# Kernel optimization log

Measured on AMD Instinct MI355X. Metric: run time of the kernel, lower is better.

The kernel has to match this reference:

```python
import jax, jax.numpy as jnp
import numpy as np
import math

B, S, DIM = 2, 2048, 2048
H, KV = 32, 8
HD = DIM // H          # 64
REP = H // KV          # 4
NEG = -1e9


def setup_inputs() -> dict:
    key = jax.random.key(0)
    ks = jax.random.split(key, 8)
    x = jax.random.normal(ks[0], (B, S, DIM), dtype=jnp.float32)
    # RoPE frequencies: theta = 10000^{-2i/d}, angles = pos * theta
    inv_freq = 1.0 / (10000.0 ** (jnp.arange(0, HD, 2, dtype=jnp.float32) / HD))  # [HD/2]
    angles = jnp.arange(S, dtype=jnp.float32)[:, None] * inv_freq[None, :]        # [S, HD/2]
    freqs_cos = jnp.cos(angles)
    freqs_sin = jnp.sin(angles)
    # additive causal mask [1,1,S,S]
    causal = jnp.tril(jnp.ones((S, S), dtype=bool))
    mask = jnp.where(causal, 0.0, NEG).astype(jnp.float32)[None, None]
    sc = 1.0 / math.sqrt(DIM)
    wq = jax.random.normal(ks[1], (DIM, H * HD), dtype=jnp.float32) * sc
    wk = jax.random.normal(ks[2], (DIM, KV * HD), dtype=jnp.float32) * sc
    wv = jax.random.normal(ks[3], (DIM, KV * HD), dtype=jnp.float32) * sc
    wo = jax.random.normal(ks[4], (H * HD, DIM), dtype=jnp.float32) * sc
    return {"x": x, "freqs_cos": freqs_cos, "freqs_sin": freqs_sin,
            "mask": mask, "wq": wq, "wk": wk, "wv": wv, "wo": wo}


def _rope(t, cos, sin):
    # t: [B,S,nh,HD]; interleaved (even, odd) pairs == view_as_complex layout
    te, to = t[..., 0::2], t[..., 1::2]
    c = cos[None, :, None, :]  # [1,S,1,HD/2]
    s = sin[None, :, None, :]
    oe = te * c - to * s
    oo = te * s + to * c
    return jnp.stack([oe, oo], axis=-1).reshape(t.shape)


def reference(x, freqs_cos, freqs_sin, mask, wq, wk, wv, wo):
    b, s, _ = x.shape
    q = (x @ wq).reshape(b, s, H, HD)
    k = (x @ wk).reshape(b, s, KV, HD)
    v = (x @ wv).reshape(b, s, KV, HD)
    q = _rope(q, freqs_cos, freqs_sin)
    k = _rope(k, freqs_cos, freqs_sin)
    # GQA without materializing repeat_interleave: group q heads by kv head
    # repeat_interleave maps query head h -> kv head h // REP
    qg = q.transpose(0, 2, 1, 3).reshape(b, KV, REP, s, HD)  # [B,KV,REP,S,HD]
    kg = k.transpose(0, 2, 1, 3)                              # [B,KV,S,HD]
    vg = v.transpose(0, 2, 1, 3)
    scores = jnp.einsum('bgrqd,bgkd->bgrqk', qg, kg) / math.sqrt(HD)
    scores = scores + mask[:, :, None]                        # [1,1,1,S,S] broadcast
    attn = jax.nn.softmax(scores, axis=-1)
    out = jnp.einsum('bgrqk,bgkd->bgrqd', attn, vg)           # [B,KV,REP,S,HD]
    out = out.reshape(b, H, s, HD).transpose(0, 2, 1, 3).reshape(b, s, H * HD)
    return out @ wo
```

## Files before the change

### kernel.cpp

```cpp
#include <hip/hip_runtime.h>
#include <hip/hip_bf16.h>

#define B_ 2
#define S_ 2048
#define DIM_ 2048
#define H_ 32
#define KV_ 8
#define HD_ 64

typedef __bf16 bf16x8 __attribute__((ext_vector_type(8)));
typedef __bf16 bf16x4 __attribute__((ext_vector_type(4)));
typedef float f32x4 __attribute__((ext_vector_type(4)));
typedef float f32x16 __attribute__((ext_vector_type(16)));
typedef unsigned u32x2 __attribute__((ext_vector_type(2)));

#define GLOAD16(gp, lp) __builtin_amdgcn_global_load_lds( \
    (const __attribute__((address_space(1))) void*)(gp),  \
    (__attribute__((address_space(3))) void*)(lp), 16, 0, 0)

__global__ __launch_bounds__(256) void cast_f32_bf16_v4(const float* __restrict__ in,
                                                        __bf16* __restrict__ out, int n4) {
    int i = blockIdx.x * 256 + threadIdx.x;
    if (i >= n4) return;
    float4 v = ((const float4*)in)[i];
    bf16x4 o;
    o[0] = (__bf16)v.x; o[1] = (__bf16)v.y; o[2] = (__bf16)v.z; o[3] = (__bf16)v.w;
    ((bf16x4*)out)[i] = o;
}

__global__ __launch_bounds__(256) void transpose_all_t(const float* __restrict__ wq,
                                                       const float* __restrict__ wk,
                                                       const float* __restrict__ wv,
                                                       const float* __restrict__ wo,
                                                       __bf16* __restrict__ wqkv_t,
                                                       __bf16* __restrict__ wo_t) {
    __shared__ float t[32][33];
    const int bk = blockIdx.x * 32, bn = blockIdx.y * 32;
    const int tx = threadIdx.x & 31, ty = threadIdx.x >> 5;
    const float* W; __bf16* Wt; int N, src;
    if (blockIdx.z == 0) {
        Wt = wqkv_t;
        if (bn < 2048)      { W = wq; N = 2048; src = bn; }
        else if (bn < 2560) { W = wk; N = 512;  src = bn - 2048; }
        else                { W = wv; N = 512;  src = bn - 2560; }
    } else {
        if (bn >= 2048) return;
        Wt = wo_t; W = wo; N = 2048; src = bn;
    }
#pragma unroll
    for (int i = 0; i < 4; i++)
        t[ty * 4 + i][tx] = W[(size_t)(bk + ty * 4 + i) * N + src + tx];
    __syncthreads();
#pragma unroll
    for (int i = 0; i < 4; i++)
        Wt[(size_t)(bn + ty * 4 + i) * 2048 + bk + tx] = (__bf16)t[tx][ty * 4 + i];
}

__global__ __launch_bounds__(512, 2)
void gemm256_qkv(const __bf16* __restrict__ A, const __bf16* __restrict__ Bt,
                 __bf16* __restrict__ q_bf, __bf16* __restrict__ k_bf,
                 __bf16* __restrict__ vt_bf,
                 const float* __restrict__ fc, const float* __restrict__ fs) {
    __shared__ __align__(16) char smem[131072];
    char* lA = smem;
    char* lB = smem + 65536;
    const int K = DIM_;
    const int tid = threadIdx.x, lane = tid & 63, wid = tid >> 6;
    const int wr2 = wid >> 2, wc2 = wid & 3;
    const int fr = lane & 15, fg = lane >> 4;
    const long i0 = (long)blockIdx.x * 256;
    const long j0 = (long)blockIdx.y * 256;

    const int r0 = tid >> 3;
    const int cc = ((tid & 7) ^ (r0 & 7)) * 8;
    const __bf16* pA = A + (i0 + r0) * (long)K + cc;
    const __bf16* pB = Bt + (j0 + r0) * (long)K + cc;
    const int NT = K >> 6;

    f32x4 acc[8][4] = {};

#define STGA(h, kt, buf) do { \
    GLOAD16(pA + (long)((h) * 128) * K + (kt) * 64,      lA + (buf) * 32768 + (h) * 16384 + tid * 16); \
    GLOAD16(pA + (long)((h) * 128 + 64) * K + (kt) * 64, lA + (buf) * 32768 + (h) * 16384 + 8192 + tid * 16); } while (0)
#define STGB(h, kt, buf) do { \
    GLOAD16(pB + (long)((h) * 128) * K + (kt) * 64,      lB + (buf) * 32768 + (h) * 16384 + tid * 16); \
    GLOAD16(pB + (long)((h) * 128 + 64) * K + (kt) * 64, lB + (buf) * 32768 + (h) * 16384 + 8192 + tid * 16); } while (0)

    STGA(0, 0, 0); STGB(0, 0, 0); STGB(1, 0, 0); STGA(1, 0, 0);

    for (int kt = 0; kt < NT; ++kt) {
        const int cur = kt & 1, nxt = cur ^ 1;
        const bool nl = (kt + 1 < NT);
        const char* cA = lA + cur * 32768;
        const char* cB = lB + cur * 32768;
        bf16x8 af[4], bfv[4];

        auto rdA = [&](int mf, int ks) -> bf16x8 {
            int row = wr2 * 128 + mf * 16 + fr;
            return *(const bf16x8*)(cA + row * 128 + (((ks << 2) | fg) ^ (row & 7)) * 16);
        };
        auto rdB = [&](int nf, int ks) -> bf16x8 {
            int row = wc2 * 64 + nf * 16 + fr;
            return *(const bf16x8*)(cB + row * 128 + (((ks << 2) | fg) ^ (row & 7)) * 16);
        };

        if (nl) { STGA(0, kt + 1, nxt); STGB(0, kt + 1, nxt); }
        if (nl) asm volatile("s_waitcnt vmcnt(4)" ::: "memory");
        else    asm volatile("s_waitcnt vmcnt(0)" ::: "memory");
        __builtin_amdgcn_s_barrier();
        asm volatile("" ::: "memory");
#pragma unroll
        for (int nf = 0; nf < 4; nf++) bfv[nf] = rdB(nf, 0);
#pragma unroll
        for (int mf = 0; mf < 4; mf++) af[mf] = rdA(mf, 0);
        __builtin_amdgcn_s_setprio(1);
#pragma unroll
        for (int mf = 0; mf < 4; mf++)
#pragma unroll
            for (int nf = 0; nf < 4; nf++)
                acc[mf][nf] = __builtin_amdgcn_mfma_f32_16x16x32_bf16(af[mf], bfv[nf], acc[mf][nf], 0, 0, 0);
        __builtin_amdgcn_s_setprio(0);
        __builtin_amdgcn_s_barrier();

#pragma unroll
        for (int mf = 0; mf < 4; mf++) af[mf] = rdA(4 + mf, 0);
        if (nl) { STGB(1, kt + 1, nxt); STGA(1, kt + 1, nxt); }
        __builtin_amdgcn_s_barrier();
        __builtin_amdgcn_s_setprio(1);
#pragma unroll
        for (int mf = 0; mf < 4; mf++)
#pragma unroll
            for (int nf = 0; nf < 4; nf++)
                acc[4 + mf][nf] = __builtin_amdgcn_mfma_f32_16x16x32_bf16(af[mf], bfv[nf], acc[4 + mf][nf], 0, 0, 0);
        __builtin_amdgcn_s_setprio(0);
        __builtin_amdgcn_s_barrier();

#pragma unroll
        for (int nf = 0; nf < 4; nf++) bfv[nf] = rdB(nf, 1);
#pragma unroll
        for (int mf = 0; mf < 4; mf++) af[mf] = rdA(mf, 1);
        __builtin_amdgcn_s_barrier();
        __builtin_amdgcn_s_setprio(1);
#pragma unroll
        for (int mf = 0; mf < 4; mf++)
#pragma unroll
            for (int nf = 0; nf < 4; nf++)
                acc[mf][nf] = __builtin_amdgcn_mfma_f32_16x16x32_bf16(af[mf], bfv[nf], acc[mf][nf], 0, 0, 0);
        __builtin_amdgcn_s_setprio(0);
        __builtin_amdgcn_s_barrier();

#pragma unroll
        for (int mf = 0; mf < 4; mf++) af[mf] = rdA(4 + mf, 1);
        __builtin_amdgcn_s_barrier();
        __builtin_amdgcn_s_setprio(1);
#pragma unroll
        for (int mf = 0; mf < 4; mf++)
#pragma unroll
            for (int nf = 0; nf < 4; nf++)
                acc[4 + mf][nf] = __builtin_amdgcn_mfma_f32_16x16x32_bf16(af[mf], bfv[nf], acc[4 + mf][nf], 0, 0, 0);
        __builtin_amdgcn_s_setprio(0);
        __builtin_amdgcn_s_barrier();
    }
#undef STGA
#undef STGB

    const long col0 = j0 + wc2 * 64;
    if (j0 < 2048) {
#pragma unroll
        for (int mf = 0; mf < 8; mf++)
#pragma unroll
            for (int nf = 0; nf < 4; nf++)
#pragma unroll
                for (int j = 0; j < 4; j++) {
                    long row = i0 + wr2 * 128 + mf * 16 + fg * 4 + j;
                    q_bf[row * 2048 + col0 + nf * 16 + fr] = (__bf16)acc[mf][nf][j];
                }
    } else if (j0 < 2560) {
#pragma unroll
        for (int mf = 0; mf < 8; mf++)
#pragma unroll
            for (int nf = 0; nf < 4; nf++) {
                const int kd = (int)(col0 + nf * 16 + fr - 2048);
                const int i_ = (kd & 63) >> 1;
                const float sgn = (fr & 1) ? 1.0f : -1.0f;
#pragma unroll
                for (int j = 0; j < 4; j++) {
                    long row = i0 + wr2 * 128 + mf * 16 + fg * 4 + j;
                    int s = (int)(row & (S_ - 1));
                    float cv = fc[s * 32 + i_], sv = fs[s * 32 + i_];
                    float v = acc[mf][nf][j];
                    float p = __shfl_xor(v, 1, 64);
                    k_bf[row * 512 + kd] = (__bf16)(v * cv + sgn * sv * p);
                }
            }
    } else {
#pragma unroll
        for (int mf = 0; mf < 8; mf++)
#pragma unroll
            for (int nf = 0; nf < 4; nf++) {
                const int vd = (int)(col0 + nf * 16 + fr - 2560);
                long row0 = i0 + wr2 * 128 + mf * 16 + fg * 4;
                int b = (int)(row0 >> 11);
                int s = (int)(row0 & (S_ - 1));
                bf16x4 pk;
#pragma unroll
                for (int j = 0; j < 4; j++) pk[j] = (__bf16)acc[mf][nf][j];
                *(bf16x4*)(vt_bf + ((size_t)(b * KV_ + (vd >> 6)) * HD_ + (vd & 63)) * S_ + s) = pk;
            }
    }
}

__global__ __launch_bounds__(512, 2)
void gemm256_o(const __bf16* __restrict__ A, const __bf16* __restrict__ Bt,
               float* __restrict__ C) {
    __shared__ __align__(16) char smem[98304];
    char* lA = smem;
    char* lB = smem + 32768;
    const int K = DIM_;
    const int tid = threadIdx.x, lane = tid & 63, wid = tid >> 6;
    const int wr2 = wid >> 2, wc2 = wid & 3;
    const int fr = lane & 15, fg = lane >> 4;
    const int id = blockIdx.x;
    const long i0 = (long)(id >> 3) * 128;
    const long j0 = (long)(id & 7) * 256;

    const int r0 = tid >> 3;
    const int cc = ((tid & 7) ^ (r0 & 7)) * 8;
    const __bf16* pA = A + (i0 + r0) * (long)K + cc;
    const __bf16* pB = Bt + (j0 + r0) * (long)K + cc;
    const int NT = K >> 6;

    f32x4 acc[4][4] = {};

#define STG(kt, buf) do { \
    GLOAD16(pA + (long)(kt) * 64,                  lA + (buf) * 16384 + tid * 16); \
    GLOAD16(pA + (long)64 * K + (long)(kt) * 64,   lA + (buf) * 16384 + 8192 + tid * 16); \
    GLOAD16(pB + (long)(kt) * 64,                  lB + (buf) * 32768 + tid * 16); \
    GLOAD16(pB + (long)64 * K + (long)(kt) * 64,   lB + (buf) * 32768 + 8192 + tid * 16); \
    GLOAD16(pB + (long)128 * K + (long)(kt) * 64,  lB + (buf) * 32768 + 16384 + tid * 16); \
    GLOAD16(pB + (long)192 * K + (long)(kt) * 64,  lB + (buf) * 32768 + 24576 + tid * 16); } while (0)

    STG(0, 0);

    for (int kt = 0; kt < NT; ++kt) {
        const int cur = kt & 1, nxt = cur ^ 1;
        const bool nl = (kt + 1 < NT);
        const char* cA = lA + cur * 16384;
        const char* cB = lB + cur * 32768;

        if (nl) STG(kt + 1, nxt);
        if (nl) asm volatile("s_waitcnt vmcnt(6)" ::: "memory");
        else    asm volatile("s_waitcnt vmcnt(0)" ::: "memory");
        __builtin_amdgcn_s_barrier();
        asm volatile("" ::: "memory");

        bf16x8 af[4], bfv[4];
#pragma unroll
        for (int ks = 0; ks < 2; ks++) {
#pragma unroll
            for (int nf = 0; nf < 4; nf++) {
                int row = wc2 * 64 + nf * 16 + fr;
                bfv[nf] = *(const bf16x8*)(cB + row * 128 + (((ks << 2) | fg) ^ (row & 7)) * 16);
            }
#pragma unroll
            for (int mf = 0; mf < 4; mf++) {
                int row = wr2 * 64 + mf * 16 + fr;
                af[mf] = *(const bf16x8*)(cA + row * 128 + (((ks << 2) | fg) ^ (row & 7)) * 16);
            }
            __builtin_amdgcn_s_setprio(1);
#pragma unroll
            for (int mf = 0; mf < 4; mf++)
#pragma unroll
                for (int nf = 0; nf < 4; nf++)
                    acc[mf][nf] = __builtin_amdgcn_mfma_f32_16x16x32_bf16(af[mf], bfv[nf], acc[mf][nf], 0, 0, 0);
            __builtin_amdgcn_s_setprio(0);
        }
        __builtin_amdgcn_s_barrier();
    }
#undef STG

#pragma unroll
    for (int mf = 0; mf < 4; mf++)
#pragma unroll
        for (int nf = 0; nf < 4; nf++)
#pragma unroll
            for (int j = 0; j < 4; j++) {
                long row = i0 + wr2 * 64 + mf * 16 + fg * 4 + j;
                long col = j0 + wc2 * 64 + nf * 16 + fr;
                C[row * 2048 + col] = acc[mf][nf][j];
            }
}

__global__ __launch_bounds__(256, 4)
void attn_fwd(const __bf16* __restrict__ Q, const __bf16* __restrict__ Kb,
              const __bf16* __restrict__ Vt, __bf16* __restrict__ O,
              const float* __restrict__ fc, const float* __restrict__ fs) {
    extern __shared__ __align__(16) char smem[];
    __bf16* lK  = (__bf16*)smem;
    __bf16* lVt = (__bf16*)(smem + 16384);

    const int tid = threadIdx.x;
    const int lane = tid & 63;
    const int wid = tid >> 6;
    const int ln = lane & 31;
    const int hi = lane >> 5;

    const int id = blockIdx.x;
    const int g = id & 7;
    const int r = id >> 3;
    const int chunk = 15 - (r >> 3);
    const int hb = r & 7;
    const int b = hb & 1;
    const int h = g * 4 + (hb >> 1);
    const int QS = H_ * HD_, KS = KV_ * HD_;
    const float K2 = 0.18033688011112042f;
    const float mK = 8.0f * K2;

    const __bf16* Kbse = Kb + (size_t)(b * S_) * KS + g * HD_;
    const __bf16* Vbse = Vt + (size_t)((b * KV_ + g) * HD_) * S_;

    bf16x8 onesf;
#pragma unroll
    for (int j = 0; j < 8; j++) onesf[j] = (__bf16)1.0f;

    const int c0 = tid, c1 = tid + 256;
    const int kr0 = c0 & 63, kd0 = c0 >> 6;
    const int kr1 = c1 & 63, kd1 = c1 >> 6;
    const __bf16* Ksrc0 = Kbse + (size_t)kr0 * KS + kd0 * 8;
    const __bf16* Ksrc1 = Kbse + (size_t)kr1 * KS + kd1 * 8;
    const __bf16* Vsrc0 = Vbse + (size_t)kr0 * S_ + kd0 * 8;
    const __bf16* Vsrc1 = Vbse + (size_t)kr1 * S_ + kd1 * 8;

    auto stage = [&](int t, int buf) {
        GLOAD16(Ksrc0 + (size_t)t * 64 * KS, lK + buf * 4096 + c0 * 8);
        GLOAD16(Ksrc1 + (size_t)t * 64 * KS, lK + buf * 4096 + c1 * 8);
        GLOAD16(Vsrc0 + t * 64,              lVt + buf * 4096 + c0 * 8);
        GLOAD16(Vsrc1 + t * 64,              lVt + buf * 4096 + c1 * 8);
    };

    const int q0w = chunk * 128 + wid * 32;
    const int qrow = q0w + ln;
    const int nt = 2 * chunk + 2;
    const int nkv_w = (q0w >> 6) + 1;

    const __bf16* Qb = Q + (size_t)(b * S_ + qrow) * QS + h * HD_;
    const float* cz = fc + (size_t)qrow * 32;
    const float* sz = fs + (size_t)qrow * 32;
    bf16x8 qf[4];
#pragma unroll
    for (int kk = 0; kk < 4; kk++) {
        bf16x8 raw = *(const bf16x8*)(Qb + kk * 16 + hi * 8);
#pragma unroll
        for (int p = 0; p < 4; p++) {
            const int i = kk * 8 + hi * 4 + p;
            float cv = cz[i], sv = sz[i];
            float e = (float)raw[2 * p], o = (float)raw[2 * p + 1];
            qf[kk][2 * p]     = (__bf16)(e * cv - o * sv);
            qf[kk][2 * p + 1] = (__bf16)(e * sv + o * cv);
        }
    }

    f32x16 o0 = {}, o1 = {}, o2 = {};

    stage(0, 0);
    __syncthreads();

    for (int t = 0; t < nt; t++) {
        if (t + 1 < nt) stage(t + 1, (t + 1) & 1);
        if (t < nkv_w) {
            const char* lKc = (const char*)(lK + (t & 1) * 4096);
            const char* lVc = (const char*)(lVt + (t & 1) * 4096);
            const int p0 = t * 64;

            f32x16 s0 = {}, s1 = {};
            __builtin_amdgcn_s_setprio(1);
#pragma unroll
            for (int kk = 0; kk < 4; kk++) {
                bf16x8 ka = *(const bf16x8*)(lKc + (kk * 2 + hi) * 1024 + ln * 16);
                s0 = __builtin_amdgcn_mfma_f32_32x32x16_bf16(ka, qf[kk], s0, 0, 0, 0);
            }
#pragma unroll
            for (int kk = 0; kk < 4; kk++) {
                bf16x8 ka = *(const bf16x8*)(lKc + (kk * 2 + hi) * 1024 + (32 + ln) * 16);
                s1 = __builtin_amdgcn_mfma_f32_32x32x16_bf16(ka, qf[kk], s1, 0, 0, 0);
            }
            __builtin_amdgcn_s_setprio(0);

            if (t == nkv_w - 1) {
#pragma unroll
                for (int rr = 0; rr < 16; rr++) {
                    int crow = (rr & 3) + 8 * (rr >> 2) + 4 * hi;
                    if (p0 + crow > qrow)      s0[rr] = -1e30f;
                    if (p0 + 32 + crow > qrow) s1[rr] = -1e30f;
                }
            }

#pragma unroll
            for (int rr = 0; rr < 16; rr++) {
                s0[rr] = exp2f(s0[rr] * K2 - mK);
                s1[rr] = exp2f(s1[rr] * K2 - mK);
            }

            __builtin_amdgcn_s_setprio(1);
#pragma unroll
            for (int c = 0; c < 2; c++) {
                const f32x16& pe = c ? s1 : s0;
                unsigned w[4][2];
#pragma unroll
                for (int gi = 0; gi < 4; gi++)
#pragma unroll
                    for (int p = 0; p < 2; p++) {
                        unsigned short lo = __builtin_bit_cast(unsigned short, (__bf16)pe[4 * gi + 2 * p]);
                        unsigned short hp = __builtin_bit_cast(unsigned short, (__bf16)pe[4 * gi + 2 * p + 1]);
                        w[gi][p] = (unsigned)lo | ((unsigned)hp << 16);
                    }
                unsigned pw0[4], pw1[4];
#pragma unroll
                for (int p = 0; p < 2; p++) {
                    u32x2 ra = __builtin_amdgcn_permlane32_swap(w[0][p], w[1][p], false, false);
                    pw0[p] = ra[0]; pw0[2 + p] = ra[1];
                    u32x2 rb = __builtin_amdgcn_permlane32_swap(w[2][p], w[3][p], false, false);
                    pw1[p] = rb[0]; pw1[2 + p] = rb[1];
                }
                bf16x8 pa0 = __builtin_bit_cast(bf16x8, *(uint4*)pw0);
                bf16x8 pa1 = __builtin_bit_cast(bf16x8, *(uint4*)pw1);
#pragma unroll
                for (int half = 0; half < 2; half++) {
                    const int ks = 2 * c + half;
                    bf16x8 pa = half ? pa1 : pa0;
                    bf16x8 va0 = *(const bf16x8*)(lVc + (ks * 2 + hi) * 1024 + ln * 16);
                    bf16x8 va1 = *(const bf16x8*)(lVc + (ks * 2 + hi) * 1024 + (32 + ln) * 16);
                    o0 = __builtin_amdgcn_mfma_f32_32x32x16_bf16(va0, pa, o0, 0, 0, 0);
                    o1 = __builtin_amdgcn_mfma_f32_32x32x16_bf16(va1, pa, o1, 0, 0, 0);
                    o2 = __builtin_amdgcn_mfma_f32_32x32x16_bf16(onesf, pa, o2, 0, 0, 0);
                }
            }
            __builtin_amdgcn_s_setprio(0);
        }
        __syncthreads();
    }

    const float inv = 1.0f / o2[0];
    __bf16* Oq = O + (size_t)(b * S_ + qrow) * QS + h * HD_;
#pragma unroll
    for (int db = 0; db < 2; db++) {
        const f32x16& oo = db ? o1 : o0;
#pragma unroll
        for (int gi = 0; gi < 4; gi++) {
            bf16x4 pk;
#pragma unroll
            for (int j = 0; j < 4; j++) pk[j] = (__bf16)(oo[4 * gi + j] * inv);
            *(bf16x4*)(Oq + db * 32 + 8 * gi + 4 * hi) = pk;
        }
    }
}

extern "C" void kernel_launch(void* const* d_in, const int* in_sizes, int n_in,
                              void* d_out, int out_size, void* d_ws, size_t ws_size,
                              hipStream_t stream) {
    const float* x  = (const float*)d_in[0];
    const float* fc = (const float*)d_in[1];
    const float* fs = (const float*)d_in[2];
    const float* wq = (const float*)d_in[4];
    const float* wk = (const float*)d_in[5];
    const float* wv = (const float*)d_in[6];
    const float* wo = (const float*)d_in[7];
    float* out = (float*)d_out;

    const size_t N0 = (size_t)B_ * S_ * DIM_;
    const size_t N1 = (size_t)B_ * S_ * H_ * HD_;
    const size_t N2 = (size_t)B_ * S_ * KV_ * HD_;
    const size_t N3 = (size_t)DIM_ * H_ * HD_;
    const size_t N4 = (size_t)DIM_ * KV_ * HD_;

    __bf16* x_bf = (__bf16*)d_ws;
    __bf16* q_bf = x_bf + N0;
    __bf16* k_bf = q_bf + N1;
    __bf16* vt_bf = k_bf + N2;
    __bf16* wqkv_t = vt_bf + N2;
    __bf16* wo_t = wqkv_t + N3 + 2 * N4;
    __bf16* ao_bf = x_bf;

    cast_f32_bf16_v4<<<dim3(N0 / 4 / 256), 256, 0, stream>>>(x, x_bf, (int)(N0 / 4));
    transpose_all_t<<<dim3(64, 96, 2), 256, 0, stream>>>(wq, wk, wv, wo, wqkv_t, wo_t);

    gemm256_qkv<<<dim3(16, 12), 512, 0, stream>>>(x_bf, wqkv_t, q_bf, k_bf, vt_bf, fc, fs);

    attn_fwd<<<dim3(1024), 256, 32768, stream>>>(q_bf, k_bf, vt_bf, ao_bf, fc, fs);

    gemm256_o<<<dim3(256), 512, 0, stream>>>(ao_bf, wo_t, out);
}
```

Measured before the change: 197.2 us.

## Load K/V tiles directly from global memory into registers in attention

Removes the LDS double-buffered staging of K and V tiles in the attention kernel. Each wave now loads its K and V MFMA operands straight from global memory into registers, so there are no block-wide barriers and each wave only loops over its own causal range. The four waves in a block share a KV head and read the same K/V rows, so this duplicates global and L2 traffic and exposes load latency without an explicit prefetch pipeline. In exchange it drops the shared-memory allocation, which may raise occupancy.

```diff
diff --git a/kernel.cpp b/kernel.cpp
--- a/kernel.cpp
+++ b/kernel.cpp
@@ -295,10 +295,6 @@
 void attn_fwd(const __bf16* __restrict__ Q, const __bf16* __restrict__ Kb,
               const __bf16* __restrict__ Vt, __bf16* __restrict__ O,
               const float* __restrict__ fc, const float* __restrict__ fs) {
-    extern __shared__ __align__(16) char smem[];
-    __bf16* lK  = (__bf16*)smem;
-    __bf16* lVt = (__bf16*)(smem + 16384);
-
     const int tid = threadIdx.x;
     const int lane = tid & 63;
     const int wid = tid >> 6;
@@ -316,31 +312,13 @@
     const float K2 = 0.18033688011112042f;
     const float mK = 8.0f * K2;
 
-    const __bf16* Kbse = Kb + (size_t)(b * S_) * KS + g * HD_;
-    const __bf16* Vbse = Vt + (size_t)((b * KV_ + g) * HD_) * S_;
-
-    bf16x8 onesf;
-#pragma unroll
-    for (int j = 0; j < 8; j++) onesf[j] = (__bf16)1.0f;
-
-    const int c0 = tid, c1 = tid + 256;
-    const int kr0 = c0 & 63, kd0 = c0 >> 6;
-    const int kr1 = c1 & 63, kd1 = c1 >> 6;
-    const __bf16* Ksrc0 = Kbse + (size_t)kr0 * KS + kd0 * 8;
-    const __bf16* Ksrc1 = Kbse + (size_t)kr1 * KS + kd1 * 8;
-    const __bf16* Vsrc0 = Vbse + (size_t)kr0 * S_ + kd0 * 8;
-    const __bf16* Vsrc1 = Vbse + (size_t)kr1 * S_ + kd1 * 8;
-
-    auto stage = [&](int t, int buf) {
-        GLOAD16(Ksrc0 + (size_t)t * 64 * KS, lK + buf * 4096 + c0 * 8);
-        GLOAD16(Ksrc1 + (size_t)t * 64 * KS, lK + buf * 4096 + c1 * 8);
-        GLOAD16(Vsrc0 + t * 64,              lVt + buf * 4096 + c0 * 8);
-        GLOAD16(Vsrc1 + t * 64,              lVt + buf * 4096 + c1 * 8);
-    };
+    const __bf16* Kl0 = Kb + (size_t)(b * S_ + ln) * KS + g * HD_ + hi * 8;
+    const __bf16* Kl1 = Kl0 + (size_t)32 * KS;
+    const __bf16* Vl0 = Vt + ((size_t)(b * KV_ + g) * HD_ + ln) * S_ + hi * 8;
+    const __bf16* Vl1 = Vl0 + (size_t)32 * S_;
 
     const int q0w = chunk * 128 + wid * 32;
     const int qrow = q0w + ln;
-    const int nt = 2 * chunk + 2;
     const int nkv_w = (q0w >> 6) + 1;
 
     const __bf16* Qb = Q + (size_t)(b * S_ + qrow) * QS + h * HD_;
@@ -360,84 +338,87 @@
         }
     }
 
+    bf16x8 onesf;
+#pragma unroll
+    for (int j = 0; j < 8; j++) onesf[j] = (__bf16)1.0f;
+
     f32x16 o0 = {}, o1 = {}, o2 = {};
 
-    stage(0, 0);
-    __syncthreads();
-
-    for (int t = 0; t < nt; t++) {
-        if (t + 1 < nt) stage(t + 1, (t + 1) & 1);
-        if (t < nkv_w) {
-            const char* lKc = (const char*)(lK + (t & 1) * 4096);
-            const char* lVc = (const char*)(lVt + (t & 1) * 4096);
-            const int p0 = t * 64;
-
-            f32x16 s0 = {}, s1 = {};
-            __builtin_amdgcn_s_setprio(1);
-#pragma unroll
-            for (int kk = 0; kk < 4; kk++) {
-                bf16x8 ka = *(const bf16x8*)(lKc + (kk * 2 + hi) * 1024 + ln * 16);
-                s0 = __builtin_amdgcn_mfma_f32_32x32x16_bf16(ka, qf[kk], s0, 0, 0, 0);
-            }
-#pragma unroll
-            for (int kk = 0; kk < 4; kk++) {
-                bf16x8 ka = *(const bf16x8*)(lKc + (kk * 2 + hi) * 1024 + (32 + ln) * 16);
-                s1 = __builtin_amdgcn_mfma_f32_32x32x16_bf16(ka, qf[kk], s1, 0, 0, 0);
-            }
-            __builtin_amdgcn_s_setprio(0);
-
-            if (t == nkv_w - 1) {
-#pragma unroll
-                for (int rr = 0; rr < 16; rr++) {
-                    int crow = (rr & 3) + 8 * (rr >> 2) + 4 * hi;
-                    if (p0 + crow > qrow)      s0[rr] = -1e30f;
-                    if (p0 + 32 + crow > qrow) s1[rr] = -1e30f;
+    for (int t = 0; t < nkv_w; t++) {
+        const int p0 = t * 64;
+
+        bf16x8 ka0[4], ka1[4];
+#pragma unroll
+        for (int kk = 0; kk < 4; kk++) {
+            ka0[kk] = *(const bf16x8*)(Kl0 + (size_t)p0 * KS + kk * 16);
+            ka1[kk] = *(const bf16x8*)(Kl1 + (size_t)p0 * KS + kk * 16);
+        }
+
+        f32x16 s0 = {}, s1 = {};
+        __builtin_amdgcn_s_setprio(1);
+#pragma unroll
+        for (int kk = 0; kk < 4; kk++)
+            s0 = __builtin_amdgcn_mfma_f32_32x32x16_bf16(ka0[kk], qf[kk], s0, 0, 0, 0);
+#pragma unroll
+        for (int kk = 0; kk < 4; kk++)
+            s1 = __builtin_amdgcn_mfma_f32_32x32x16_bf16(ka1[kk], qf[kk], s1, 0, 0, 0);
+        __builtin_amdgcn_s_setprio(0);
+
+        bf16x8 va[4][2];
+#pragma unroll
+        for (int ks = 0; ks < 4; ks++) {
+            va[ks][0] = *(const bf16x8*)(Vl0 + p0 + ks * 16);
+            va[ks][1] = *(const bf16x8*)(Vl1 + p0 + ks * 16);
+        }
+
+        if (t == nkv_w - 1) {
+#pragma unroll
+            for (int rr = 0; rr < 16; rr++) {
+                int crow = (rr & 3) + 8 * (rr >> 2) + 4 * hi;
+                if (p0 + crow > qrow)      s0[rr] = -1e30f;
+                if (p0 + 32 + crow > qrow) s1[rr] = -1e30f;
+            }
+        }
+
+#pragma unroll
+        for (int rr = 0; rr < 16; rr++) {
+            s0[rr] = exp2f(s0[rr] * K2 - mK);
+            s1[rr] = exp2f(s1[rr] * K2 - mK);
+        }
+
+        __builtin_amdgcn_s_setprio(1);
+#pragma unroll
+        for (int c = 0; c < 2; c++) {
+            const f32x16& pe = c ? s1 : s0;
+            unsigned w[4][2];
+#pragma unroll
+            for (int gi = 0; gi < 4; gi++)
+#pragma unroll
+                for (int p = 0; p < 2; p++) {
+                    unsigned short lo = __builtin_bit_cast(unsigned short, (__bf16)pe[4 * gi + 2 * p]);
+                    unsigned short hp = __builtin_bit_cast(unsigned short, (__bf16)pe[4 * gi + 2 * p + 1]);
+                    w[gi][p] = (unsigned)lo | ((unsigned)hp << 16);
                 }
-            }
-
-#pragma unroll
-            for (int rr = 0; rr < 16; rr++) {
-                s0[rr] = exp2f(s0[rr] * K2 - mK);
-                s1[rr] = exp2f(s1[rr] * K2 - mK);
-            }
-
-            __builtin_amdgcn_s_setprio(1);
-#pragma unroll
-            for (int c = 0; c < 2; c++) {
-                const f32x16& pe = c ? s1 : s0;
-                unsigned w[4][2];
-#pragma unroll
-                for (int gi = 0; gi < 4; gi++)
-#pragma unroll
-                    for (int p = 0; p < 2; p++) {
-                        unsigned short lo = __builtin_bit_cast(unsigned short, (__bf16)pe[4 * gi + 2 * p]);
-                        unsigned short hp = __builtin_bit_cast(unsigned short, (__bf16)pe[4 * gi + 2 * p + 1]);
-                        w[gi][p] = (unsigned)lo | ((unsigned)hp << 16);
-                    }
-                unsigned pw0[4], pw1[4];
-#pragma unroll
-                for (int p = 0; p < 2; p++) {
-                    u32x2 ra = __builtin_amdgcn_permlane32_swap(w[0][p], w[1][p], false, false);
-                    pw0[p] = ra[0]; pw0[2 + p] = ra[1];
-                    u32x2 rb = __builtin_amdgcn_permlane32_swap(w[2][p], w[3][p], false, false);
-                    pw1[p] = rb[0]; pw1[2 + p] = rb[1];
-                }
-                bf16x8 pa0 = __builtin_bit_cast(bf16x8, *(uint4*)pw0);
-                bf16x8 pa1 = __builtin_bit_cast(bf16x8, *(uint4*)pw1);
-#pragma unroll
-                for (int half = 0; half < 2; half++) {
-                    const int ks = 2 * c + half;
-                    bf16x8 pa = half ? pa1 : pa0;
-                    bf16x8 va0 = *(const bf16x8*)(lVc + (ks * 2 + hi) * 1024 + ln * 16);
-                    bf16x8 va1 = *(const bf16x8*)(lVc + (ks * 2 + hi) * 1024 + (32 + ln) * 16);
-                    o0 = __builtin_amdgcn_mfma_f32_32x32x16_bf16(va0, pa, o0, 0, 0, 0);
-                    o1 = __builtin_amdgcn_mfma_f32_32x32x16_bf16(va1, pa, o1, 0, 0, 0);
-                    o2 = __builtin_amdgcn_mfma_f32_32x32x16_bf16(onesf, pa, o2, 0, 0, 0);
-                }
-            }
-            __builtin_amdgcn_s_setprio(0);
-        }
-        __syncthreads();
+            unsigned pw0[4], pw1[4];
+#pragma unroll
+            for (int p = 0; p < 2; p++) {
+                u32x2 ra = __builtin_amdgcn_permlane32_swap(w[0][p], w[1][p], false, false);
+                pw0[p] = ra[0]; pw0[2 + p] = ra[1];
+                u32x2 rb = __builtin_amdgcn_permlane32_swap(w[2][p], w[3][p], false, false);
+                pw1[p] = rb[0]; pw1[2 + p] = rb[1];
+            }
+            bf16x8 pa0 = __builtin_bit_cast(bf16x8, *(uint4*)pw0);
+            bf16x8 pa1 = __builtin_bit_cast(bf16x8, *(uint4*)pw1);
+#pragma unroll
+            for (int half = 0; half < 2; half++) {
+                const int ks = 2 * c + half;
+                bf16x8 pa = half ? pa1 : pa0;
+                o0 = __builtin_amdgcn_mfma_f32_32x32x16_bf16(va[ks][0], pa, o0, 0, 0, 0);
+                o1 = __builtin_amdgcn_mfma_f32_32x32x16_bf16(va[ks][1], pa, o1, 0, 0, 0);
+                o2 = __builtin_amdgcn_mfma_f32_32x32x16_bf16(onesf, pa, o2, 0, 0, 0);
+            }
+        }
+        __builtin_amdgcn_s_setprio(0);
     }
 
     const float inv = 1.0f / o2[0];
@@ -486,7 +467,7 @@
 
     gemm256_qkv<<<dim3(16, 12), 512, 0, stream>>>(x_bf, wqkv_t, q_bf, k_bf, vt_bf, fc, fs);
 
-    attn_fwd<<<dim3(1024), 256, 32768, stream>>>(q_bf, k_bf, vt_bf, ao_bf, fc, fs);
+    attn_fwd<<<dim3(1024), 256, 0, stream>>>(q_bf, k_bf, vt_bf, ao_bf, fc, fs);
 
     gemm256_o<<<dim3(256), 512, 0, stream>>>(ao_bf, wo_t, out);
 }
```

After: 332.7 us. 1.69x slower.
